# Kernel tuning notes

Measured on AMD Instinct MI355X. Metric: run time of the kernel, lower is better.

Reference implementation:

```python
import jax, jax.numpy as jnp
import numpy as np


def normalize_adj(adj):
    """Symmetrize (adj + adj.T*(adj.T>adj) - adj*(adj.T>adj)), add self loops, row-normalize D^-1 A."""
    at = jnp.swapaxes(adj, -1, -2)
    mask = (at > adj).astype(adj.dtype)
    a = adj + at * mask - adj * mask
    m = a.shape[-1]
    a = a + jnp.eye(m, dtype=a.dtype)
    rowsum = a.sum(axis=-1, keepdims=True)
    inv = jnp.where(rowsum > 0, 1.0 / rowsum, 0.0)
    return a * inv


def setup_inputs() -> dict:
    key = jax.random.key(0)
    ks = jax.random.split(key, 8)
    N, n, T, dim, M = 4, 3, 512, 2048, 256
    x = jax.random.normal(ks[0], (N, n, T, dim), dtype=jnp.float32)
    nodes = jax.random.normal(ks[1], (N, M, dim), dtype=jnp.float32)
    adj = (jax.random.uniform(ks[2], (N, M, M)) < 0.05).astype(jnp.float32)
    conv_w = jax.random.normal(ks[3], (2048, dim, 3), dtype=jnp.float32) * 0.02  # OIH
    conv_b = jnp.zeros((2048,), dtype=jnp.float32)
    W1 = jax.random.normal(ks[4], (dim, dim), dtype=jnp.float32) * 0.02
    b1 = jnp.zeros((dim,), dtype=jnp.float32)
    W2 = jax.random.normal(ks[5], (dim, dim), dtype=jnp.float32) * 0.02
    b2 = jnp.zeros((dim,), dtype=jnp.float32)
    return {"x": x, "nodes": nodes, "adj": adj, "conv_w": conv_w, "conv_b": conv_b,
            "W1": W1, "b1": b1, "W2": W2, "b2": b2}


def reference(x, nodes, adj, conv_w, conv_b, W1, b1, W2, b2):
    N, n, T, dim = x.shape
    # Conv1d front-end: (N*n, C=dim, T), kernel 3, pad 1, then ReLU
    feats = x.reshape(N * n, T, dim).transpose(0, 2, 1)  # [B, C, T]
    feats = jax.lax.conv_general_dilated(
        feats, conv_w, window_strides=(1,), padding=[(1, 1)],
        dimension_numbers=("NCH", "OIH", "NCH"))
    feats = jax.nn.relu(feats + conv_b[None, :, None])
    feats = feats.transpose(0, 2, 1).reshape(N, n, T, dim)
    # GCN_Module over per-sample node graphs (batched over N)
    a = normalize_adj(adj)                                   # [N, M, M]
    h = jax.nn.relu(jnp.einsum("bij,bjf->bif", a, nodes @ W1) + b1)
    out = jnp.einsum("bij,bjf->bif", a, h @ W2) + b2         # [N, M, dim]
    return feats, out
```

## Files before the change

kernel.cpp:

```cpp
#include <hip/hip_runtime.h>
#include <stdint.h>

typedef __bf16 bf16x8 __attribute__((ext_vector_type(8)));
typedef float floatx4 __attribute__((ext_vector_type(4)));

__device__ __forceinline__ void gload_lds16(const void* g, void* l) {
    __builtin_amdgcn_global_load_lds((const __attribute__((address_space(1))) void*)g,
                                     (__attribute__((address_space(3))) void*)l, 16, 0, 0);
}

__device__ __forceinline__ uint16_t f2bf(float f) {
    uint32_t u = __float_as_uint(f);
    u += 0x7fff + ((u >> 16) & 1);
    return (uint16_t)(u >> 16);
}
__device__ __forceinline__ uint32_t f2bf2(float lo, float hi) {
    return (uint32_t)f2bf(lo) | ((uint32_t)f2bf(hi) << 16);
}

struct AmulSM {
    float vv[256];
    int   jj[256];
    float part[4];
    int   wcnt[4];
    int   woff[4];
    float sinv;
    int   n0;
};

__device__ __forceinline__ void amul_body(const float* __restrict__ adj,
                                          const float* __restrict__ H,
                                          uint16_t* __restrict__ outp,
                                          int b, int i, int tid, AmulSM* sm)
{
    const float* A = adj + ((size_t)b << 16);
    float aij = A[(i << 8) + tid];
    float aji = A[(tid << 8) + i];
    float v = fmaxf(aij, aji);
    if (tid == i) v += 1.0f;

    float s = v;
    #pragma unroll
    for (int off = 32; off > 0; off >>= 1) s += __shfl_down(s, off);

    bool pred = v != 0.0f;
    unsigned long long m = __ballot(pred);
    int wid = tid >> 6;
    if ((tid & 63) == 0) { sm->part[wid] = s; sm->wcnt[wid] = (int)__popcll(m); }
    __syncthreads();
    if (tid == 0) {
        float t = sm->part[0] + sm->part[1] + sm->part[2] + sm->part[3];
        sm->sinv = t > 0.0f ? 1.0f / t : 0.0f;
        int o = 0;
        #pragma unroll
        for (int w = 0; w < 4; ++w) { sm->woff[w] = o; o += sm->wcnt[w]; }
        sm->n0 = o;
    }
    __syncthreads();
    if (pred) {
        int pos = sm->woff[wid] + (int)__popcll(m & ((1ull << (tid & 63)) - 1ull));
        sm->vv[pos] = v * sm->sinv;
        sm->jj[pos] = tid;
    }
    __syncthreads();

    const int n0 = sm->n0;
    const int f0 = tid * 8;
    const float* Hb = H + (((size_t)b) << 8) * 2048;
    float acc[8] = {};
    for (int c = 0; c < n0; ++c) {
        float av = sm->vv[c];
        const float* hp = Hb + (size_t)sm->jj[c] * 2048 + f0;
        float4 p = *(const float4*)hp;
        float4 q = *(const float4*)(hp + 4);
        acc[0] += av * p.x; acc[1] += av * p.y; acc[2] += av * p.z; acc[3] += av * p.w;
        acc[4] += av * q.x; acc[5] += av * q.y; acc[6] += av * q.z; acc[7] += av * q.w;
    }
    uint4 o;
    o.x = f2bf2(acc[0], acc[1]);
    o.y = f2bf2(acc[2], acc[3]);
    o.z = f2bf2(acc[4], acc[5]);
    o.w = f2bf2(acc[6], acc[7]);
    *(uint4*)(outp + (((size_t)b << 8) + i) * 2048 + f0) = o;
}

__device__ __forceinline__ void amul_swizzle(int bid, int& b, int& i) {
    int x = bid & 7, g = bid >> 3;
    b = x >> 1;
    i = ((x & 1) << 7) + g;
}

#define PR_AM 1024
#define PR_W  3072
#define PR_T  4096
#define PR_N  28768

__global__ __launch_bounds__(256)
void k_prep(const float* __restrict__ x, uint32_t* __restrict__ xpad,
            const float* __restrict__ w, uint16_t* __restrict__ wT,
            const float* __restrict__ W1, uint16_t* __restrict__ W1T,
            const float* __restrict__ adj, const float* __restrict__ nodes,
            uint16_t* __restrict__ gbf)
{
    __shared__ union {
        float  wbuf[6144];
        float  tile[64][65];
        AmulSM am;
    } sm;
    const int bid = blockIdx.x;
    const int tid = threadIdx.x;

    if (bid < PR_AM) {
        int b, i; amul_swizzle(bid, b, i);
        amul_body(adj, nodes, gbf, b, i, tid, &sm.am);
    } else if (bid < PR_W) {
        int o = bid - PR_AM;
        const float* src = w + (size_t)o * 6144;
        uint16_t*    dst = wT + (size_t)o * 6144;
        #pragma unroll
        for (int it = 0; it < 24; ++it)
            sm.wbuf[it * 256 + tid] = src[it * 256 + tid];
        __syncthreads();
        #pragma unroll
        for (int h = 0; h < 3; ++h)
            #pragma unroll
            for (int c = 0; c < 8; ++c) {
                int i = c * 256 + tid;
                dst[h * 2048 + i] = f2bf(sm.wbuf[i * 3 + h]);
            }
    } else if (bid < PR_T) {
        int t  = bid - PR_W;
        int by = (t >> 5) & 31;
        int bx = t & 31;
        int tx = tid & 63, ty = tid >> 6;
        for (int rr = ty; rr < 64; rr += 4)
            sm.tile[rr][tx] = W1[(size_t)(by * 64 + rr) * 2048 + bx * 64 + tx];
        __syncthreads();
        for (int rr = ty; rr < 64; rr += 4)
            W1T[(size_t)(bx * 64 + rr) * 2048 + by * 64 + tx] = f2bf(sm.tile[tx][rr]);
    } else {
        int idx2 = (bid - PR_T) * 256 + tid;
        int i2   = idx2 & 1023;
        int tmp  = idx2 >> 10;
        int b    = tmp / 514;
        int tt   = tmp - b * 514;
        float2 v = {0.0f, 0.0f};
        if (tt >= 1 && tt <= 512)
            v = *(const float2*)(x + ((size_t)(b * 512 + tt - 1) << 11) + i2 * 2);
        xpad[idx2] = f2bf2(v.x, v.y);
    }
}

__global__ __launch_bounds__(256)
void k_big(const uint16_t* __restrict__ xpad, const uint16_t* __restrict__ wmT,
           float* __restrict__ feats, const float* __restrict__ conv_b,
           const uint16_t* __restrict__ gbf, const uint16_t* __restrict__ W1T,
           float* __restrict__ h, const float* __restrict__ b1,
           const float* __restrict__ W2, uint16_t* __restrict__ W2T)
{
    __shared__ __align__(16) union {
        uint16_t u16[8192];
        float    tile[64][65];
    } sm;
    const int bid  = blockIdx.x;
    const int tid  = threadIdx.x;
    const int lane = tid & 63;
    const int wave = tid >> 6;
    const int lm   = lane & 15;
    const int kq   = (lane >> 4) * 8;
    const int lq   = lane >> 4;
    const int srow  = tid >> 2;
    const int skcol = (tid & 3) * 8;

    if (bid < 768) {
        uint16_t* As = sm.u16;
        uint16_t* Bs = sm.u16 + 4096;
        const int xc = bid & 7;
        const int g  = bid >> 3;
        const int rt = (12 * (xc >> 1) + (g % 12)) * 128;
        const int ct = (8 * (xc & 1) + (g / 12)) * 128;
        const int wm = (wave >> 1) * 64;
        const int wn = (wave & 1) * 64;

        floatx4 acc[4][4] = {};

        for (int k0 = 0; k0 < 6144; k0 += 32) {
            #pragma unroll
            for (int ii = 0; ii < 2; ++ii) {
                int row = ii * 64 + srow;
                int r  = rt + row;
                int b  = r >> 9;
                int t  = r & 511;
                int kk = k0 + skcol;
                int hh = kk >> 11;
                int ic = kk & 2047;
                gload_lds16(xpad + ((size_t)(b * 514 + t + hh) << 11) + ic,
                            &As[ii * 2048 + tid * 8]);
                gload_lds16(wmT + (size_t)(ct + row) * 6144 + k0 + skcol,
                            &Bs[ii * 2048 + tid * 8]);
            }
            __syncthreads();

            bf16x8 af[4], bfr[4];
            #pragma unroll
            for (int mt = 0; mt < 4; ++mt)
                af[mt] = *(const bf16x8*)&As[(wm + mt * 16 + lm) * 32 + kq];
            #pragma unroll
            for (int nt = 0; nt < 4; ++nt)
                bfr[nt] = *(const bf16x8*)&Bs[(wn + nt * 16 + lm) * 32 + kq];
            #pragma unroll
            for (int mt = 0; mt < 4; ++mt)
                #pragma unroll
                for (int nt = 0; nt < 4; ++nt)
                    acc[mt][nt] = __builtin_amdgcn_mfma_f32_16x16x32_bf16(af[mt], bfr[nt], acc[mt][nt], 0, 0, 0);
            __syncthreads();
        }

        #pragma unroll
        for (int mt = 0; mt < 4; ++mt)
            #pragma unroll
            for (int nt = 0; nt < 4; ++nt) {
                int col = ct + wn + nt * 16 + lm;
                float bv = conv_b[col];
                #pragma unroll
                for (int r = 0; r < 4; ++r) {
                    int row = rt + wm + mt * 16 + lq * 4 + r;
                    feats[(size_t)row * 2048 + col] = fmaxf(acc[mt][nt][r] + bv, 0.0f);
                }
            }
    } else if (bid < 1280) {
        uint16_t* As = sm.u16;
        uint16_t* Bs = sm.u16 + 2048;
        const int t  = bid - 768;
        const int xc = t & 7;
        const int g  = t >> 3;
        const int rt = (g & 15) * 64;
        const int ct = (4 * xc + (g >> 4)) * 64;
        const int wm = (wave >> 1) * 32;
        const int wn = (wave & 1) * 32;

        const size_t abase = (size_t)(rt + srow) * 2048 + skcol;
        const size_t bbase = (size_t)(ct + srow) * 2048 + skcol;

        floatx4 acc[2][2] = {};

        for (int k0 = 0; k0 < 2048; k0 += 32) {
            gload_lds16(gbf + abase + k0, &As[tid * 8]);
            gload_lds16(W1T + bbase + k0, &Bs[tid * 8]);
            __syncthreads();

            bf16x8 af[2], bfr[2];
            #pragma unroll
            for (int mt = 0; mt < 2; ++mt)
                af[mt] = *(const bf16x8*)&As[(wm + mt * 16 + lm) * 32 + kq];
            #pragma unroll
            for (int nt = 0; nt < 2; ++nt)
                bfr[nt] = *(const bf16x8*)&Bs[(wn + nt * 16 + lm) * 32 + kq];
            #pragma unroll
            for (int mt = 0; mt < 2; ++mt)
                #pragma unroll
                for (int nt = 0; nt < 2; ++nt)
                    acc[mt][nt] = __builtin_amdgcn_mfma_f32_16x16x32_bf16(af[mt], bfr[nt], acc[mt][nt], 0, 0, 0);
            __syncthreads();
        }

        #pragma unroll
        for (int mt = 0; mt < 2; ++mt)
            #pragma unroll
            for (int nt = 0; nt < 2; ++nt) {
                int col = ct + wn + nt * 16 + lm;
                float bv = b1[col];
                #pragma unroll
                for (int r = 0; r < 4; ++r) {
                    int row = rt + wm + mt * 16 + lq * 4 + r;
                    h[(size_t)row * 2048 + col] = fmaxf(acc[mt][nt][r] + bv, 0.0f);
                }
            }
    } else {
        int t  = bid - 1280;
        int by = (t >> 5) & 31;
        int bx = t & 31;
        int tx = tid & 63, ty = tid >> 6;
        for (int rr = ty; rr < 64; rr += 4)
            sm.tile[rr][tx] = W2[(size_t)(by * 64 + rr) * 2048 + bx * 64 + tx];
        __syncthreads();
        for (int rr = ty; rr < 64; rr += 4)
            W2T[(size_t)(bx * 64 + rr) * 2048 + by * 64 + tx] = f2bf(sm.tile[tx][rr]);
    }
}

__global__ __launch_bounds__(256)
void k_amul(const float* __restrict__ adj, const float* __restrict__ H,
            uint16_t* __restrict__ outp)
{
    __shared__ AmulSM sm;
    int b, i; amul_swizzle(blockIdx.x, b, i);
    amul_body(adj, H, outp, b, i, threadIdx.x, &sm);
}

__global__ __launch_bounds__(256)
void k_gemm64(const uint16_t* __restrict__ A, const uint16_t* __restrict__ BT,
              float* __restrict__ C, const float* __restrict__ bias)
{
    __shared__ __align__(16) uint16_t As[64 * 32];
    __shared__ __align__(16) uint16_t Bs[64 * 32];
    const int tid  = threadIdx.x;
    const int bid  = blockIdx.x;
    const int xc   = bid & 7;
    const int g    = bid >> 3;
    const int rt   = (g & 15) * 64;
    const int ct   = (4 * xc + (g >> 4)) * 64;
    const int lane = tid & 63;
    const int wave = tid >> 6;
    const int wm   = (wave >> 1) * 32;
    const int wn   = (wave & 1) * 32;
    const int lm   = lane & 15;
    const int kq   = (lane >> 4) * 8;
    const int srow  = tid >> 2;
    const int skcol = (tid & 3) * 8;

    const size_t abase = (size_t)(rt + srow) * 2048 + skcol;
    const size_t bbase = (size_t)(ct + srow) * 2048 + skcol;

    floatx4 acc[2][2] = {};

    for (int k0 = 0; k0 < 2048; k0 += 32) {
        gload_lds16(A  + abase + k0, &As[tid * 8]);
        gload_lds16(BT + bbase + k0, &Bs[tid * 8]);
        __syncthreads();

        bf16x8 af[2], bfr[2];
        #pragma unroll
        for (int mt = 0; mt < 2; ++mt)
            af[mt] = *(const bf16x8*)&As[(wm + mt * 16 + lm) * 32 + kq];
        #pragma unroll
        for (int nt = 0; nt < 2; ++nt)
            bfr[nt] = *(const bf16x8*)&Bs[(wn + nt * 16 + lm) * 32 + kq];
        #pragma unroll
        for (int mt = 0; mt < 2; ++mt)
            #pragma unroll
            for (int nt = 0; nt < 2; ++nt)
                acc[mt][nt] = __builtin_amdgcn_mfma_f32_16x16x32_bf16(af[mt], bfr[nt], acc[mt][nt], 0, 0, 0);
        __syncthreads();
    }

    const int lq = lane >> 4;
    #pragma unroll
    for (int mt = 0; mt < 2; ++mt)
        #pragma unroll
        for (int nt = 0; nt < 2; ++nt) {
            int col = ct + wn + nt * 16 + lm;
            float bv = bias[col];
            #pragma unroll
            for (int r = 0; r < 4; ++r) {
                int row = rt + wm + mt * 16 + lq * 4 + r;
                C[(size_t)row * 2048 + col] = acc[mt][nt][r] + bv;
            }
        }
}


extern "C" void kernel_launch(void* const* d_in, const int* in_sizes, int n_in,
                              void* d_out, int out_size, void* d_ws, size_t ws_size,
                              hipStream_t stream)
{
    const float* x      = (const float*)d_in[0];
    const float* nodes  = (const float*)d_in[1];
    const float* adj    = (const float*)d_in[2];
    const float* conv_w = (const float*)d_in[3];
    const float* conv_b = (const float*)d_in[4];
    const float* W1     = (const float*)d_in[5];
    const float* b1     = (const float*)d_in[6];
    const float* W2     = (const float*)d_in[7];
    const float* b2     = (const float*)d_in[8];
    float* out = (float*)d_out;

    char* ws = (char*)d_ws;
    uint16_t* xpad   = (uint16_t*)(ws);
    uint16_t* wmT    = (uint16_t*)(ws + 25288704);
    uint16_t* W1T    = (uint16_t*)(ws + 50454528);
    uint16_t* W2T    = (uint16_t*)(ws + 58843136);
    uint16_t* gbf    = (uint16_t*)(ws + 67231744);
    float*    h      = (float*)   (ws + 71426048);
    uint16_t* ahb    = (uint16_t*)(ws + 79814656);

    k_prep<<<PR_N, 256, 0, stream>>>(x, (uint32_t*)xpad, conv_w, wmT,
                                     W1, W1T, adj, nodes, gbf);
    k_big<<<2304, 256, 0, stream>>>(xpad, wmT, out, conv_b, gbf, W1T, h, b1, W2, W2T);
    k_amul<<<1024, 256, 0, stream>>>(adj, h, ahb);
    k_gemm64<<<512, 256, 0, stream>>>(ahb, W2T, out + 12582912, b2);
}
```

Baseline: 431.4 us.

## Fuse all stages into one persistent kernel with atomic-counter dependencies

```diff
diff --git a/kernel.cpp b/kernel.cpp
--- a/kernel.cpp
+++ b/kernel.cpp
@@ -16,6 +16,18 @@
 }
 __device__ __forceinline__ uint32_t f2bf2(float lo, float hi) {
     return (uint32_t)f2bf(lo) | ((uint32_t)f2bf(hi) << 16);
+}
+
+__device__ __forceinline__ void bump(int* p) {
+    __syncthreads();
+    if (threadIdx.x == 0)
+        __hip_atomic_fetch_add(p, 1, __ATOMIC_RELEASE, __HIP_MEMORY_SCOPE_AGENT);
+}
+__device__ __forceinline__ void wait_ge(int* p, int target) {
+    if (threadIdx.x == 0)
+        while (__hip_atomic_load(p, __ATOMIC_ACQUIRE, __HIP_MEMORY_SCOPE_AGENT) < target)
+            __builtin_amdgcn_s_sleep(2);
+    __syncthreads();
 }
 
 struct AmulSM {
@@ -26,6 +38,13 @@
     int   woff[4];
     float sinv;
     int   n0;
+};
+
+union MegaSM {
+    uint16_t u16[8192];
+    float    wbuf[6144];
+    float    tile[64][65];
+    AmulSM   am;
 };
 
 __device__ __forceinline__ void amul_body(const float* __restrict__ adj,
@@ -84,230 +103,23 @@
     *(uint4*)(outp + (((size_t)b << 8) + i) * 2048 + f0) = o;
 }
 
-__device__ __forceinline__ void amul_swizzle(int bid, int& b, int& i) {
-    int x = bid & 7, g = bid >> 3;
+__device__ __forceinline__ void amul_swizzle(int id, int& b, int& i) {
+    int x = id & 7, g = id >> 3;
     b = x >> 1;
     i = ((x & 1) << 7) + g;
 }
 
-#define PR_AM 1024
-#define PR_W  3072
-#define PR_T  4096
-#define PR_N  28768
-
-__global__ __launch_bounds__(256)
-void k_prep(const float* __restrict__ x, uint32_t* __restrict__ xpad,
-            const float* __restrict__ w, uint16_t* __restrict__ wT,
-            const float* __restrict__ W1, uint16_t* __restrict__ W1T,
-            const float* __restrict__ adj, const float* __restrict__ nodes,
-            uint16_t* __restrict__ gbf)
+template<bool RELU>
+__device__ __forceinline__ void g64_tile(MegaSM* sm, const uint16_t* __restrict__ A,
+                                         const uint16_t* __restrict__ BT,
+                                         float* __restrict__ C, const float* __restrict__ bias,
+                                         int id)
 {
-    __shared__ union {
-        float  wbuf[6144];
-        float  tile[64][65];
-        AmulSM am;
-    } sm;
-    const int bid = blockIdx.x;
-    const int tid = threadIdx.x;
-
-    if (bid < PR_AM) {
-        int b, i; amul_swizzle(bid, b, i);
-        amul_body(adj, nodes, gbf, b, i, tid, &sm.am);
-    } else if (bid < PR_W) {
-        int o = bid - PR_AM;
-        const float* src = w + (size_t)o * 6144;
-        uint16_t*    dst = wT + (size_t)o * 6144;
-        #pragma unroll
-        for (int it = 0; it < 24; ++it)
-            sm.wbuf[it * 256 + tid] = src[it * 256 + tid];
-        __syncthreads();
-        #pragma unroll
-        for (int h = 0; h < 3; ++h)
-            #pragma unroll
-            for (int c = 0; c < 8; ++c) {
-                int i = c * 256 + tid;
-                dst[h * 2048 + i] = f2bf(sm.wbuf[i * 3 + h]);
-            }
-    } else if (bid < PR_T) {
-        int t  = bid - PR_W;
-        int by = (t >> 5) & 31;
-        int bx = t & 31;
-        int tx = tid & 63, ty = tid >> 6;
-        for (int rr = ty; rr < 64; rr += 4)
-            sm.tile[rr][tx] = W1[(size_t)(by * 64 + rr) * 2048 + bx * 64 + tx];
-        __syncthreads();
-        for (int rr = ty; rr < 64; rr += 4)
-            W1T[(size_t)(bx * 64 + rr) * 2048 + by * 64 + tx] = f2bf(sm.tile[tx][rr]);
-    } else {
-        int idx2 = (bid - PR_T) * 256 + tid;
-        int i2   = idx2 & 1023;
-        int tmp  = idx2 >> 10;
-        int b    = tmp / 514;
-        int tt   = tmp - b * 514;
-        float2 v = {0.0f, 0.0f};
-        if (tt >= 1 && tt <= 512)
-            v = *(const float2*)(x + ((size_t)(b * 512 + tt - 1) << 11) + i2 * 2);
-        xpad[idx2] = f2bf2(v.x, v.y);
-    }
-}
-
-__global__ __launch_bounds__(256)
-void k_big(const uint16_t* __restrict__ xpad, const uint16_t* __restrict__ wmT,
-           float* __restrict__ feats, const float* __restrict__ conv_b,
-           const uint16_t* __restrict__ gbf, const uint16_t* __restrict__ W1T,
-           float* __restrict__ h, const float* __restrict__ b1,
-           const float* __restrict__ W2, uint16_t* __restrict__ W2T)
-{
-    __shared__ __align__(16) union {
-        uint16_t u16[8192];
-        float    tile[64][65];
-    } sm;
-    const int bid  = blockIdx.x;
+    uint16_t* As = sm->u16;
+    uint16_t* Bs = sm->u16 + 2048;
     const int tid  = threadIdx.x;
-    const int lane = tid & 63;
-    const int wave = tid >> 6;
-    const int lm   = lane & 15;
-    const int kq   = (lane >> 4) * 8;
-    const int lq   = lane >> 4;
-    const int srow  = tid >> 2;
-    const int skcol = (tid & 3) * 8;
-
-    if (bid < 768) {
-        uint16_t* As = sm.u16;
-        uint16_t* Bs = sm.u16 + 4096;
-        const int xc = bid & 7;
-        const int g  = bid >> 3;
-        const int rt = (12 * (xc >> 1) + (g % 12)) * 128;
-        const int ct = (8 * (xc & 1) + (g / 12)) * 128;
-        const int wm = (wave >> 1) * 64;
-        const int wn = (wave & 1) * 64;
-
-        floatx4 acc[4][4] = {};
-
-        for (int k0 = 0; k0 < 6144; k0 += 32) {
-            #pragma unroll
-            for (int ii = 0; ii < 2; ++ii) {
-                int row = ii * 64 + srow;
-                int r  = rt + row;
-                int b  = r >> 9;
-                int t  = r & 511;
-                int kk = k0 + skcol;
-                int hh = kk >> 11;
-                int ic = kk & 2047;
-                gload_lds16(xpad + ((size_t)(b * 514 + t + hh) << 11) + ic,
-                            &As[ii * 2048 + tid * 8]);
-                gload_lds16(wmT + (size_t)(ct + row) * 6144 + k0 + skcol,
-                            &Bs[ii * 2048 + tid * 8]);
-            }
-            __syncthreads();
-
-            bf16x8 af[4], bfr[4];
-            #pragma unroll
-            for (int mt = 0; mt < 4; ++mt)
-                af[mt] = *(const bf16x8*)&As[(wm + mt * 16 + lm) * 32 + kq];
-            #pragma unroll
-            for (int nt = 0; nt < 4; ++nt)
-                bfr[nt] = *(const bf16x8*)&Bs[(wn + nt * 16 + lm) * 32 + kq];
-            #pragma unroll
-            for (int mt = 0; mt < 4; ++mt)
-                #pragma unroll
-                for (int nt = 0; nt < 4; ++nt)
-                    acc[mt][nt] = __builtin_amdgcn_mfma_f32_16x16x32_bf16(af[mt], bfr[nt], acc[mt][nt], 0, 0, 0);
-            __syncthreads();
-        }
-
-        #pragma unroll
-        for (int mt = 0; mt < 4; ++mt)
-            #pragma unroll
-            for (int nt = 0; nt < 4; ++nt) {
-                int col = ct + wn + nt * 16 + lm;
-                float bv = conv_b[col];
-                #pragma unroll
-                for (int r = 0; r < 4; ++r) {
-                    int row = rt + wm + mt * 16 + lq * 4 + r;
-                    feats[(size_t)row * 2048 + col] = fmaxf(acc[mt][nt][r] + bv, 0.0f);
-                }
-            }
-    } else if (bid < 1280) {
-        uint16_t* As = sm.u16;
-        uint16_t* Bs = sm.u16 + 2048;
-        const int t  = bid - 768;
-        const int xc = t & 7;
-        const int g  = t >> 3;
-        const int rt = (g & 15) * 64;
-        const int ct = (4 * xc + (g >> 4)) * 64;
-        const int wm = (wave >> 1) * 32;
-        const int wn = (wave & 1) * 32;
-
-        const size_t abase = (size_t)(rt + srow) * 2048 + skcol;
-        const size_t bbase = (size_t)(ct + srow) * 2048 + skcol;
-
-        floatx4 acc[2][2] = {};
-
-        for (int k0 = 0; k0 < 2048; k0 += 32) {
-            gload_lds16(gbf + abase + k0, &As[tid * 8]);
-            gload_lds16(W1T + bbase + k0, &Bs[tid * 8]);
-            __syncthreads();
-
-            bf16x8 af[2], bfr[2];
-            #pragma unroll
-            for (int mt = 0; mt < 2; ++mt)
-                af[mt] = *(const bf16x8*)&As[(wm + mt * 16 + lm) * 32 + kq];
-            #pragma unroll
-            for (int nt = 0; nt < 2; ++nt)
-                bfr[nt] = *(const bf16x8*)&Bs[(wn + nt * 16 + lm) * 32 + kq];
-            #pragma unroll
-            for (int mt = 0; mt < 2; ++mt)
-                #pragma unroll
-                for (int nt = 0; nt < 2; ++nt)
-                    acc[mt][nt] = __builtin_amdgcn_mfma_f32_16x16x32_bf16(af[mt], bfr[nt], acc[mt][nt], 0, 0, 0);
-            __syncthreads();
-        }
-
-        #pragma unroll
-        for (int mt = 0; mt < 2; ++mt)
-            #pragma unroll
-            for (int nt = 0; nt < 2; ++nt) {
-                int col = ct + wn + nt * 16 + lm;
-                float bv = b1[col];
-                #pragma unroll
-                for (int r = 0; r < 4; ++r) {
-                    int row = rt + wm + mt * 16 + lq * 4 + r;
-                    h[(size_t)row * 2048 + col] = fmaxf(acc[mt][nt][r] + bv, 0.0f);
-                }
-            }
-    } else {
-        int t  = bid - 1280;
-        int by = (t >> 5) & 31;
-        int bx = t & 31;
-        int tx = tid & 63, ty = tid >> 6;
-        for (int rr = ty; rr < 64; rr += 4)
-            sm.tile[rr][tx] = W2[(size_t)(by * 64 + rr) * 2048 + bx * 64 + tx];
-        __syncthreads();
-        for (int rr = ty; rr < 64; rr += 4)
-            W2T[(size_t)(bx * 64 + rr) * 2048 + by * 64 + tx] = f2bf(sm.tile[tx][rr]);
-    }
-}
-
-__global__ __launch_bounds__(256)
-void k_amul(const float* __restrict__ adj, const float* __restrict__ H,
-            uint16_t* __restrict__ outp)
-{
-    __shared__ AmulSM sm;
-    int b, i; amul_swizzle(blockIdx.x, b, i);
-    amul_body(adj, H, outp, b, i, threadIdx.x, &sm);
-}
-
-__global__ __launch_bounds__(256)
-void k_gemm64(const uint16_t* __restrict__ A, const uint16_t* __restrict__ BT,
-              float* __restrict__ C, const float* __restrict__ bias)
-{
-    __shared__ __align__(16) uint16_t As[64 * 32];
-    __shared__ __align__(16) uint16_t Bs[64 * 32];
-    const int tid  = threadIdx.x;
-    const int bid  = blockIdx.x;
-    const int xc   = bid & 7;
-    const int g    = bid >> 3;
+    const int xc   = id & 7;
+    const int g    = id >> 3;
     const int rt   = (g & 15) * 64;
     const int ct   = (4 * xc + (g >> 4)) * 64;
     const int lane = tid & 63;
@@ -354,9 +166,164 @@
             #pragma unroll
             for (int r = 0; r < 4; ++r) {
                 int row = rt + wm + mt * 16 + lq * 4 + r;
-                C[(size_t)row * 2048 + col] = acc[mt][nt][r] + bv;
+                float v = acc[mt][nt][r] + bv;
+                if (RELU) v = fmaxf(v, 0.0f);
+                C[(size_t)row * 2048 + col] = v;
             }
         }
+}
+
+struct KP {
+    const float *x, *nodes, *adj, *conv_w, *conv_b, *W1, *b1, *W2, *b2;
+    uint16_t *xpad, *wmT, *W1T, *W2T, *gbf, *ahb;
+    float *h, *feats, *out2;
+    int *cnt0, *cntH, *cnt2;
+};
+
+#define IT_AM 1024
+#define IT_W  3072
+#define IT_T1 4096
+#define IT_T2 5120
+#define IT_N  17456
+
+__global__ __launch_bounds__(256, 3) void k_mega(KP p)
+{
+    __shared__ MegaSM sm;
+    const int bid  = blockIdx.x;
+    const int tid  = threadIdx.x;
+    const int lane = tid & 63;
+    const int wave = tid >> 6;
+    const int lm   = lane & 15;
+    const int kq   = (lane >> 4) * 8;
+    const int lq   = lane >> 4;
+    const int srow  = tid >> 2;
+    const int skcol = (tid & 3) * 8;
+
+    for (int item = bid; item < IT_N; item += 768) {
+        if (item < IT_AM) {
+            int b, i; amul_swizzle(item, b, i);
+            amul_body(p.adj, p.nodes, p.gbf, b, i, tid, &sm.am);
+        } else if (item < IT_W) {
+            int o = item - IT_AM;
+            const float* src = p.conv_w + (size_t)o * 6144;
+            uint16_t*    dst = p.wmT + (size_t)o * 6144;
+            #pragma unroll
+            for (int it = 0; it < 24; ++it)
+                sm.wbuf[it * 256 + tid] = src[it * 256 + tid];
+            __syncthreads();
+            #pragma unroll
+            for (int hh = 0; hh < 3; ++hh)
+                #pragma unroll
+                for (int c = 0; c < 8; ++c) {
+                    int i = c * 256 + tid;
+                    dst[hh * 2048 + i] = f2bf(sm.wbuf[i * 3 + hh]);
+                }
+        } else if (item < IT_T2) {
+            int t  = item - ((item < IT_T1) ? IT_W : IT_T1);
+            const float* src = (item < IT_T1) ? p.W1 : p.W2;
+            uint16_t*    dst = (item < IT_T1) ? p.W1T : p.W2T;
+            int by = (t >> 5) & 31;
+            int bx = t & 31;
+            int tx = tid & 63, ty = tid >> 6;
+            for (int rr = ty; rr < 64; rr += 4)
+                sm.tile[rr][tx] = src[(size_t)(by * 64 + rr) * 2048 + bx * 64 + tx];
+            __syncthreads();
+            for (int rr = ty; rr < 64; rr += 4)
+                dst[(size_t)(bx * 64 + rr) * 2048 + by * 64 + tx] = f2bf(sm.tile[tx][rr]);
+        } else {
+            int idx4 = (item - IT_T2) * 256 + tid;
+            int ch4  = idx4 & 511;
+            int tmp  = idx4 >> 9;
+            int b    = tmp / 514;
+            int tt   = tmp - b * 514;
+            float4 v = {0.0f, 0.0f, 0.0f, 0.0f};
+            if (tt >= 1 && tt <= 512)
+                v = *(const float4*)(p.x + ((size_t)(b * 512 + tt - 1) << 11) + ch4 * 4);
+            uint2 o = { f2bf2(v.x, v.y), f2bf2(v.z, v.w) };
+            ((uint2*)p.xpad)[idx4] = o;
+        }
+        __syncthreads();
+    }
+    bump(p.cnt0);
+    wait_ge(p.cnt0, 768);
+
+    {
+        uint16_t* As = sm.u16;
+        uint16_t* Bs = sm.u16 + 4096;
+        const int xc = bid & 7;
+        const int g  = bid >> 3;
+        const int rt = (12 * (xc >> 1) + (g % 12)) * 128;
+        const int ct = (8 * (xc & 1) + (g / 12)) * 128;
+        const int wm = (wave >> 1) * 64;
+        const int wn = (wave & 1) * 64;
+
+        floatx4 acc[4][4] = {};
+
+        for (int k0 = 0; k0 < 6144; k0 += 32) {
+            #pragma unroll
+            for (int ii = 0; ii < 2; ++ii) {
+                int row = ii * 64 + srow;
+                int r  = rt + row;
+                int b  = r >> 9;
+                int t  = r & 511;
+                int kk = k0 + skcol;
+                int hh = kk >> 11;
+                int ic = kk & 2047;
+                gload_lds16(p.xpad + ((size_t)(b * 514 + t + hh) << 11) + ic,
+                            &As[ii * 2048 + tid * 8]);
+                gload_lds16(p.wmT + (size_t)(ct + row) * 6144 + k0 + skcol,
+                            &Bs[ii * 2048 + tid * 8]);
+            }
+            __syncthreads();
+
+            bf16x8 af[4], bfr[4];
+            #pragma unroll
+            for (int mt = 0; mt < 4; ++mt)
+                af[mt] = *(const bf16x8*)&As[(wm + mt * 16 + lm) * 32 + kq];
+            #pragma unroll
+            for (int nt = 0; nt < 4; ++nt)
+                bfr[nt] = *(const bf16x8*)&Bs[(wn + nt * 16 + lm) * 32 + kq];
+            #pragma unroll
+            for (int mt = 0; mt < 4; ++mt)
+                #pragma unroll
+                for (int nt = 0; nt < 4; ++nt)
+                    acc[mt][nt] = __builtin_amdgcn_mfma_f32_16x16x32_bf16(af[mt], bfr[nt], acc[mt][nt], 0, 0, 0);
+            __syncthreads();
+        }
+
+        #pragma unroll
+        for (int mt = 0; mt < 4; ++mt)
+            #pragma unroll
+            for (int nt = 0; nt < 4; ++nt) {
+                int col = ct + wn + nt * 16 + lm;
+                float bv = p.conv_b[col];
+                #pragma unroll
+                for (int r = 0; r < 4; ++r) {
+                    int row = rt + wm + mt * 16 + lq * 4 + r;
+                    p.feats[(size_t)row * 2048 + col] = fmaxf(acc[mt][nt][r] + bv, 0.0f);
+                }
+            }
+    }
+
+    if (bid < 512) {
+        g64_tile<true>(&sm, p.gbf, p.W1T, p.h, p.b1, bid);
+        bump(&p.cntH[((bid >> 3) & 15) >> 2]);
+    }
+    {
+        wait_ge(&p.cntH[bid >> 8], 128);
+        amul_body(p.adj, p.h, p.ahb, bid >> 8, bid & 255, tid, &sm.am);
+        bump(&p.cnt2[bid >> 6]);
+    }
+    if (bid < 256) {
+        wait_ge(&p.cntH[3], 128);
+        amul_body(p.adj, p.h, p.ahb, 3, bid, tid, &sm.am);
+        bump(&p.cnt2[12 + (bid >> 6)]);
+    }
+    if (bid >= 256) {
+        int id = bid - 256;
+        wait_ge(&p.cnt2[(id >> 3) & 15], 64);
+        g64_tile<false>(&sm, p.ahb, p.W2T, p.out2, p.b2, id);
+    }
 }
 
 
@@ -364,29 +331,30 @@
                               void* d_out, int out_size, void* d_ws, size_t ws_size,
                               hipStream_t stream)
 {
-    const float* x      = (const float*)d_in[0];
-    const float* nodes  = (const float*)d_in[1];
-    const float* adj    = (const float*)d_in[2];
-    const float* conv_w = (const float*)d_in[3];
-    const float* conv_b = (const float*)d_in[4];
-    const float* W1     = (const float*)d_in[5];
-    const float* b1     = (const float*)d_in[6];
-    const float* W2     = (const float*)d_in[7];
-    const float* b2     = (const float*)d_in[8];
-    float* out = (float*)d_out;
-
     char* ws = (char*)d_ws;
-    uint16_t* xpad   = (uint16_t*)(ws);
-    uint16_t* wmT    = (uint16_t*)(ws + 25288704);
-    uint16_t* W1T    = (uint16_t*)(ws + 50454528);
-    uint16_t* W2T    = (uint16_t*)(ws + 58843136);
-    uint16_t* gbf    = (uint16_t*)(ws + 67231744);
-    float*    h      = (float*)   (ws + 71426048);
-    uint16_t* ahb    = (uint16_t*)(ws + 79814656);
-
-    k_prep<<<PR_N, 256, 0, stream>>>(x, (uint32_t*)xpad, conv_w, wmT,
-                                     W1, W1T, adj, nodes, gbf);
-    k_big<<<2304, 256, 0, stream>>>(xpad, wmT, out, conv_b, gbf, W1T, h, b1, W2, W2T);
-    k_amul<<<1024, 256, 0, stream>>>(adj, h, ahb);
-    k_gemm64<<<512, 256, 0, stream>>>(ahb, W2T, out + 12582912, b2);
-}
+    KP p;
+    p.x      = (const float*)d_in[0];
+    p.nodes  = (const float*)d_in[1];
+    p.adj    = (const float*)d_in[2];
+    p.conv_w = (const float*)d_in[3];
+    p.conv_b = (const float*)d_in[4];
+    p.W1     = (const float*)d_in[5];
+    p.b1     = (const float*)d_in[6];
+    p.W2     = (const float*)d_in[7];
+    p.b2     = (const float*)d_in[8];
+    p.xpad   = (uint16_t*)(ws);
+    p.wmT    = (uint16_t*)(ws + 25288704);
+    p.W1T    = (uint16_t*)(ws + 50454528);
+    p.W2T    = (uint16_t*)(ws + 58843136);
+    p.gbf    = (uint16_t*)(ws + 67231744);
+    p.h      = (float*)   (ws + 71426048);
+    p.ahb    = (uint16_t*)(ws + 79814656);
+    p.cnt0   = (int*)     (ws + 84008960);
+    p.cntH   = p.cnt0 + 1;
+    p.cnt2   = p.cnt0 + 5;
+    p.feats  = (float*)d_out;
+    p.out2   = (float*)d_out + 12582912;
+
+    hipMemsetAsync(p.cnt0, 0, 128, stream);
+    k_mega<<<768, 256, 0, stream>>>(p);
+}
```

Result: slower. 913.8 us (+111.8%).
